# Performance work log

Measured on AMD Instinct MI355X. Metric: run time of the kernel, lower is better.

Reference implementation:

```python
import jax, jax.numpy as jnp
import numpy as np

N_NODES, N_EDGES = 50000, 800000
D_H, D_E, HID = 128, 64, 128  # dim_in = D_H + D_E = 192; hidden_dim2 = D_H + HID = 256


def setup_inputs() -> dict:
    key = jax.random.key(0)
    k1, k2, k3, k4, k5 = jax.random.split(key, 5)
    H = jax.random.normal(k1, (N_NODES, D_H), dtype=jnp.float32)
    idx = jax.random.randint(k2, (2, N_EDGES), 0, N_NODES)
    X_e = jax.random.normal(k3, (N_EDGES, D_E), dtype=jnp.float32)
    # kaiming_normal (fan_in mode, relu gain): std = sqrt(2 / fan_in)
    W1 = jax.random.normal(k4, (D_H + D_E, HID), dtype=jnp.float32) * np.sqrt(2.0 / (D_H + D_E)).astype(np.float32)
    W2 = jax.random.normal(k5, (D_H + HID, HID), dtype=jnp.float32) * np.sqrt(2.0 / (D_H + HID)).astype(np.float32)
    return {"H": H, "idx": idx, "X_e": X_e, "W1": W1, "W2": W2}


def reference(H, idx, X_e, W1, W2):
    # gather source-node embeddings and concat with edge features: [E, d_h + d_e]
    x = jnp.concatenate([H[idx[0]], X_e], axis=1)
    y = jax.nn.relu(x @ W1)                                   # [E, HID]
    # scatter_max into destination nodes; empty segments -> 0 (torch_scatter zero fill).
    y = jax.ops.segment_max(y, idx[1], num_segments=H.shape[0])
    y = jnp.maximum(y, 0.0)  # relu output >= 0, so this only fixes -inf empties
    y = jnp.concatenate([H, y], axis=1)                       # [N, d_h + HID]
    y = jax.nn.relu(y @ W2)                                   # [N, HID]
    return y + H  # residual connection (HID == d_h)
```

## Files before the change

### kernel.cpp

```cpp
#include <hip/hip_runtime.h>
#include <hip/hip_bf16.h>
#include <stdint.h>

#define N_NODES 50000
#define N_EDGES 800000
#define D_H 128
#define D_E 64
#define HID 128

#define MTILE 96
#define SMAX 16
#define N_ETILES ((N_EDGES + MTILE - 1) / MTILE)

#define SCAN_B 512
#define N_CHUNKS ((N_NODES + SCAN_B - 1) / SCAN_B)

typedef __attribute__((ext_vector_type(8))) short bf16x8;
typedef __attribute__((ext_vector_type(4))) short s16x4;
typedef __attribute__((ext_vector_type(4))) float f32x4;
typedef __attribute__((ext_vector_type(4))) int i32x4;

__device__ __forceinline__ unsigned short f2bf(float x) {
    unsigned int u = __float_as_uint(x);
    u += 0x7FFFu + ((u >> 16) & 1u);
    return (unsigned short)(u >> 16);
}

__device__ __forceinline__ bf16x8 pack8(const f32x4 a, const f32x4 b) {
    bf16x8 o = { (short)f2bf(a[0]), (short)f2bf(a[1]), (short)f2bf(a[2]), (short)f2bf(a[3]),
                 (short)f2bf(b[0]), (short)f2bf(b[1]), (short)f2bf(b[2]), (short)f2bf(b[3]) };
    return o;
}

#define NG4 (N_NODES * HID / 4)
#define ND4 (N_NODES / 4)
__global__ void zero_ws(float* __restrict__ gmax, int* __restrict__ deg) {
    const int i = blockIdx.x * blockDim.x + threadIdx.x;
    if (i < NG4) {
        ((f32x4*)gmax)[i] = f32x4{0.f, 0.f, 0.f, 0.f};
    } else if (i < NG4 + ND4) {
        ((i32x4*)deg)[i - NG4] = i32x4{0, 0, 0, 0};
    }
}

#define NHB4 (N_NODES * D_H / 4)
#define NW1 (192 * HID)
#define NW2 (256 * HID)
__global__ void conv_aux(const float* __restrict__ H,
                         const float* __restrict__ W1,
                         const float* __restrict__ W2,
                         unsigned short* __restrict__ Hb,
                         unsigned short* __restrict__ W1t,
                         unsigned short* __restrict__ W2t) {
    const int i = blockIdx.x * blockDim.x + threadIdx.x;
    if (i < NHB4) {
        const f32x4 v = ((const f32x4*)H)[i];
        s16x4 pkv = { (short)f2bf(v[0]), (short)f2bf(v[1]),
                      (short)f2bf(v[2]), (short)f2bf(v[3]) };
        ((s16x4*)Hb)[i] = pkv;
    } else if (i < NHB4 + NW1) {
        const int j = i - NHB4;
        const int n = j / 192, k = j - n * 192;
        W1t[j] = f2bf(W1[k * HID + n]);
    } else if (i < NHB4 + NW1 + NW2) {
        const int j = i - NHB4 - NW1;
        const int n = j >> 8, k = j & 255;
        W2t[j] = f2bf(W2[k * HID + n]);
    }
}

__global__ void hist(const int* __restrict__ idx, int* __restrict__ deg) {
    const int i = blockIdx.x * blockDim.x + threadIdx.x;
    atomicAdd(&deg[idx[N_EDGES + i]], 1);
}

__global__ void scan_a(const int* __restrict__ deg, int* __restrict__ sc,
                       int* __restrict__ totals) {
    __shared__ int s[SCAN_B];
    const int tid = threadIdx.x;
    const int i = blockIdx.x * SCAN_B + tid;
    const int v = (i < N_NODES) ? deg[i] : 0;
    s[tid] = v;
    __syncthreads();
    for (int o = 1; o < SCAN_B; o <<= 1) {
        int t = (tid >= o) ? s[tid - o] : 0;
        __syncthreads();
        s[tid] += t;
        __syncthreads();
    }
    if (i < N_NODES) sc[i] = s[tid] - v;
    if (tid == SCAN_B - 1) totals[blockIdx.x] = s[SCAN_B - 1];
}

__global__ void scan_b(int* __restrict__ totals) {
    __shared__ int s[128];
    const int tid = threadIdx.x;
    const int v = (tid < N_CHUNKS) ? totals[tid] : 0;
    s[tid] = v;
    __syncthreads();
    for (int o = 1; o < 128; o <<= 1) {
        int t = (tid >= o) ? s[tid - o] : 0;
        __syncthreads();
        s[tid] += t;
        __syncthreads();
    }
    if (tid < N_CHUNKS) totals[tid] = s[tid] - v;
}

__global__ void scan_c(const int* __restrict__ sc, const int* __restrict__ totals,
                       int* __restrict__ cursor) {
    const int i = blockIdx.x * SCAN_B + threadIdx.x;
    if (i < N_NODES) cursor[i] = sc[i] + totals[blockIdx.x];
}

__global__ void scatter(const int* __restrict__ idx, int* __restrict__ cursor,
                        unsigned long long* __restrict__ pk8) {
    int i = blockIdx.x * blockDim.x + threadIdx.x;
    const int s = idx[i];
    const int d = idx[N_EDGES + i];
    const int p = atomicAdd(&cursor[d], 1);
    pk8[p] = (unsigned long long)(unsigned)i |
             ((unsigned long long)(unsigned)s << 20) |
             ((unsigned long long)(unsigned)d << 37);
}

__global__ __launch_bounds__(512, 6)
void edge_sorted(const float* __restrict__ H,
                 const unsigned short* __restrict__ Hb,
                 const float* __restrict__ Xe,
                 const float* __restrict__ W1,
                 const unsigned short* __restrict__ W1t,
                 const unsigned long long* __restrict__ pk8,
                 float* __restrict__ gmax, int useAux) {
    __shared__ unsigned short sX[MTILE][200];
    __shared__ float ymax[SMAX + 1][132];
    __shared__ int rowD[MTILE];
    __shared__ int segNode[SMAX];
    __shared__ int sWaveTot[8];
    __shared__ unsigned char rowG[MTILE];

    const int tid  = threadIdx.x;
    const int wave = tid >> 6;
    const int lane = tid & 63;
    const int p0   = blockIdx.x * MTILE;

    const int col = lane & 15;
    const int kr0 = (lane >> 4) * 8;

    if (useAux) {
        #pragma unroll
        for (int it = 0; it < 3; ++it) {
            const int j   = tid + it * 512;
            const int row = j >> 4;
            const int c8  = (j & 15) * 8;
            int pe = p0 + row; if (pe >= N_EDGES) pe = N_EDGES - 1;
            const int src = (int)((pk8[pe] >> 20) & 0x1FFFFull);
            *(bf16x8*)&sX[row][c8] = *(const bf16x8*)(Hb + (size_t)src * D_H + c8);
        }
    } else {
        #pragma unroll
        for (int it = 0; it < 6; ++it) {
            const int j   = tid + it * 512;
            const int row = j >> 5;
            const int c4  = (j & 31) * 4;
            int pe = p0 + row; if (pe >= N_EDGES) pe = N_EDGES - 1;
            const int src = (int)((pk8[pe] >> 20) & 0x1FFFFull);
            const f32x4 v = *(const f32x4*)(H + (size_t)src * D_H + c4);
            s16x4 pkv = { (short)f2bf(v[0]), (short)f2bf(v[1]),
                          (short)f2bf(v[2]), (short)f2bf(v[3]) };
            *(s16x4*)&sX[row][c4] = pkv;
        }
    }
    #pragma unroll
    for (int it = 0; it < 2; ++it) {
        const int j = tid + it * 512;
        if (j < 768) {
            const int row = j >> 3;
            const int c8  = (j & 7) * 8;
            int pe = p0 + row; if (pe >= N_EDGES) pe = N_EDGES - 1;
            const int e = (int)(pk8[pe] & 0xFFFFFull);
            const float* p = Xe + (size_t)e * D_E + c8;
            *(bf16x8*)&sX[row][128 + c8] = pack8(*(const f32x4*)p, *(const f32x4*)(p + 4));
        }
    }

    const int ncol = wave * 16 + col;
    bf16x8 bfrag[6];
    if (useAux) {
        #pragma unroll
        for (int ks = 0; ks < 6; ++ks)
            bfrag[ks] = *(const bf16x8*)&W1t[(size_t)ncol * 192 + ks * 32 + kr0];
    } else {
        #pragma unroll
        for (int ks = 0; ks < 6; ++ks) {
            const int kb = ks * 32 + kr0;
            bf16x8 b;
            #pragma unroll
            for (int f = 0; f < 8; ++f) b[f] = (short)f2bf(W1[(kb + f) * HID + ncol]);
            bfrag[ks] = b;
        }
    }

    const int pe0 = p0 + tid;
    const bool inTile = (tid < MTILE);
    const bool valid  = inTile && (pe0 < N_EDGES);
    int d = 0;
    if (inTile) {
        const int pc = valid ? pe0 : (N_EDGES - 1);
        d = (int)(pk8[pc] >> 37);
        rowD[tid] = d;
    }
    int dp = __shfl_up(d, 1);
    if (lane == 0 && inTile && tid > 0) dp = (int)(pk8[pe0 - 1] >> 37);
    const bool flag = valid && (tid == 0 || d != dp);
    const unsigned long long m = __ballot(flag);
    if (lane == 0) sWaveTot[wave] = (int)__popcll(m);

    for (int i2 = tid; i2 < (SMAX + 1) * 132; i2 += 512) ((float*)ymax)[i2] = 0.f;
    __syncthreads();

    int g = 255;
    if (valid) {
        const unsigned long long le =
            (lane == 63) ? ~0ull : ((1ull << (lane + 1)) - 1);
        g = (int)__popcll(m & le) - 1 + ((wave == 1) ? sWaveTot[0] : 0);
    }
    if (inTile) rowG[tid] = (unsigned char)(valid ? g : 255);
    if (flag && g < SMAX) segNode[g] = d;
    __syncthreads();

    f32x4 acc[6];
    #pragma unroll
    for (int mm = 0; mm < 6; ++mm) acc[mm] = f32x4{0.f, 0.f, 0.f, 0.f};
    const int arow = lane & 15;
    __builtin_amdgcn_s_setprio(1);
    #pragma unroll
    for (int ks = 0; ks < 6; ++ks)
        #pragma unroll
        for (int mm = 0; mm < 6; ++mm) {
            bf16x8 a = *(const bf16x8*)&sX[mm * 16 + arow][ks * 32 + kr0];
            acc[mm] = __builtin_amdgcn_mfma_f32_16x16x32_bf16(a, bfrag[ks], acc[mm], 0, 0, 0);
        }
    __builtin_amdgcn_s_setprio(0);

    const int rb = (lane >> 4) * 4;
    const int cb = wave * 16 + col;
    #pragma unroll
    for (int mm = 0; mm < 6; ++mm) {
        const int r0 = mm * 16 + rb;
        const int g0 = rowG[r0];
        const int g3 = rowG[r0 + 3];
        if (g0 == g3) {
            const float v0 = fmaxf(fmaxf(acc[mm][0], acc[mm][1]),
                                   fmaxf(acc[mm][2], acc[mm][3]));
            if (g0 < SMAX) {
                if (v0 > 0.f) atomicMax((int*)&ymax[g0][cb], __float_as_int(v0));
            } else if (g0 < 255) {
                if (v0 > 0.f)
                    atomicMax((int*)(gmax + (size_t)rowD[r0] * HID + cb), __float_as_int(v0));
            }
        } else {
            #pragma unroll
            for (int r = 0; r < 4; ++r) {
                const int gg = rowG[r0 + r];
                const float v0 = acc[mm][r];
                if (gg < SMAX) {
                    if (v0 > 0.f) atomicMax((int*)&ymax[gg][cb], __float_as_int(v0));
                } else if (gg < 255) {
                    if (v0 > 0.f)
                        atomicMax((int*)(gmax + (size_t)rowD[r0 + r] * HID + cb), __float_as_int(v0));
                }
            }
        }
    }
    __syncthreads();

    const int nSeg = sWaveTot[0] + sWaveTot[1];
    const int nS = (nSeg < SMAX) ? nSeg : SMAX;
    for (int i2 = tid; i2 < nS * 128; i2 += 512) {
        const int sg = i2 >> 7;
        const int c  = i2 & 127;
        const float v = ymax[sg][c];
        float* dst = gmax + (size_t)segNode[sg] * HID + c;
        if (sg == 0 || sg == nSeg - 1) {
            if (v > 0.f) atomicMax((int*)dst, __float_as_int(v));
        } else {
            *dst = v;
        }
    }
}

__global__ __launch_bounds__(256, 4)
void node_mlp(const float* __restrict__ H,
              const float* __restrict__ gmax,
              const float* __restrict__ W2,
              const unsigned short* __restrict__ W2t,
              float* __restrict__ out, int useAux) {
    __shared__ unsigned short sA[64][264];

    const int tid  = threadIdx.x;
    const int wave = tid >> 6;
    const int lane = tid & 63;
    const int base = blockIdx.x * 64;

    const int col = lane & 15;
    const int kr0 = (lane >> 4) * 8;
    bf16x8 bfrag[8][2];
    if (useAux) {
        #pragma unroll
        for (int ks = 0; ks < 8; ++ks)
            #pragma unroll
            for (int nf = 0; nf < 2; ++nf) {
                const int n = wave * 32 + nf * 16 + col;
                bfrag[ks][nf] = *(const bf16x8*)&W2t[(size_t)n * 256 + ks * 32 + kr0];
            }
    } else {
        #pragma unroll
        for (int ks = 0; ks < 8; ++ks)
            #pragma unroll
            for (int nf = 0; nf < 2; ++nf) {
                const int n  = wave * 32 + nf * 16 + col;
                const int kb = ks * 32 + kr0;
                bf16x8 b;
                #pragma unroll
                for (int f = 0; f < 8; ++f) b[f] = (short)f2bf(W2[(kb + f) * HID + n]);
                bfrag[ks][nf] = b;
            }
    }

    #pragma unroll
    for (int it = 0; it < 8; ++it) {
        const int i   = tid + it * 256;
        const int row = i >> 5;
        const int c4  = (i & 31) * 4;
        int node = base + row;
        if (node >= N_NODES) node = N_NODES - 1;
        const f32x4 v = *(const f32x4*)(H + (size_t)node * D_H + c4);
        s16x4 pkv = { (short)f2bf(v[0]), (short)f2bf(v[1]),
                      (short)f2bf(v[2]), (short)f2bf(v[3]) };
        *(s16x4*)&sA[row][c4] = pkv;
    }
    #pragma unroll
    for (int it = 0; it < 8; ++it) {
        const int i   = tid + it * 256;
        const int row = i >> 5;
        const int c4  = (i & 31) * 4;
        int node = base + row;
        if (node >= N_NODES) node = N_NODES - 1;
        const f32x4 v = *(const f32x4*)(gmax + (size_t)node * HID + c4);
        s16x4 pkv = { (short)f2bf(v[0]), (short)f2bf(v[1]),
                      (short)f2bf(v[2]), (short)f2bf(v[3]) };
        *(s16x4*)&sA[row][128 + c4] = pkv;
    }
    __syncthreads();

    f32x4 acc[4][2];
    #pragma unroll
    for (int mm = 0; mm < 4; ++mm) {
        acc[mm][0] = f32x4{0.f, 0.f, 0.f, 0.f};
        acc[mm][1] = f32x4{0.f, 0.f, 0.f, 0.f};
    }
    const int arow = lane & 15;
    __builtin_amdgcn_s_setprio(1);
    #pragma unroll
    for (int ks = 0; ks < 8; ++ks)
        #pragma unroll
        for (int mm = 0; mm < 4; ++mm) {
            bf16x8 a = *(const bf16x8*)&sA[mm * 16 + arow][ks * 32 + kr0];
            acc[mm][0] = __builtin_amdgcn_mfma_f32_16x16x32_bf16(a, bfrag[ks][0], acc[mm][0], 0, 0, 0);
            acc[mm][1] = __builtin_amdgcn_mfma_f32_16x16x32_bf16(a, bfrag[ks][1], acc[mm][1], 0, 0, 0);
        }
    __builtin_amdgcn_s_setprio(0);

    const int rb = (lane >> 4) * 4;
    #pragma unroll
    for (int mm = 0; mm < 4; ++mm)
        #pragma unroll
        for (int r = 0; r < 4; ++r) {
            const int node = base + mm * 16 + rb + r;
            if (node < N_NODES) {
                const size_t o = (size_t)node * HID + wave * 32 + col;
                out[o]      = fmaxf(acc[mm][0][r], 0.f) + H[o];
                out[o + 16] = fmaxf(acc[mm][1][r], 0.f) + H[o + 16];
            }
        }
}

extern "C" void kernel_launch(void* const* d_in, const int* in_sizes, int n_in,
                              void* d_out, int out_size, void* d_ws, size_t ws_size,
                              hipStream_t stream) {
    const float* H   = (const float*)d_in[0];
    const int*   idx = (const int*)d_in[1];
    const float* Xe  = (const float*)d_in[2];
    const float* W1  = (const float*)d_in[3];
    const float* W2  = (const float*)d_in[4];
    float* out = (float*)d_out;

    char* ws = (char*)d_ws;
    float* gmax   = (float*)(ws);
    int*   deg    = (int*)(ws + 25600000);
    int*   sc     = (int*)(ws + 25800192);
    int*   totals = (int*)(ws + 26000384);
    unsigned long long* pk8 = (unsigned long long*)(ws + 26000896);
    unsigned short* W1t = (unsigned short*)(ws + 32400896);
    unsigned short* W2t = (unsigned short*)(ws + 32450048);
    unsigned short* Hb  = (unsigned short*)(ws + 32515584);
    const int useAux = (ws_size >= (size_t)45315584) ? 1 : 0;

    zero_ws<<<(NG4 + ND4 + 255) / 256, 256, 0, stream>>>(gmax, deg);
    if (useAux)
        conv_aux<<<(NHB4 + NW1 + NW2 + 255) / 256, 256, 0, stream>>>(H, W1, W2, Hb, W1t, W2t);
    hist<<<N_EDGES / 256, 256, 0, stream>>>(idx, deg);
    scan_a<<<N_CHUNKS, SCAN_B, 0, stream>>>(deg, sc, totals);
    scan_b<<<1, 128, 0, stream>>>(totals);
    scan_c<<<N_CHUNKS, SCAN_B, 0, stream>>>(sc, totals, deg);
    scatter<<<N_EDGES / 256, 256, 0, stream>>>(idx, deg, pk8);
    edge_sorted<<<N_ETILES, 512, 0, stream>>>(H, Hb, Xe, W1, W1t, pk8, gmax, useAux);
    node_mlp<<<(N_NODES + 63) / 64, 256, 0, stream>>>(H, gmax, W2, W2t, out, useAux);
}
```

Baseline: 258.3 us.

## Make edge kernel persistent over four tiles with register-prefetched gathers

Each edge_sorted block now processes four consecutive 96-edge tiles instead of one. Edge metadata is double-buffered in shared memory, and the gathers of H/Xe rows for the next tile are issued into registers while the current tile's MFMA and scatter-max run. W1 fragment loads and the LDS setup are amortized across tiles. The change adds register pressure (launch bounds lowered to 4 waves per SIMD), extra syncs per tile, and a quarter as many blocks, which may reduce parallelism.

```diff
diff --git a/kernel.cpp b/kernel.cpp
--- a/kernel.cpp
+++ b/kernel.cpp
@@ -11,6 +11,8 @@
 #define MTILE 96
 #define SMAX 16
 #define N_ETILES ((N_EDGES + MTILE - 1) / MTILE)
+#define TPB 4
+#define N_EBLK ((N_ETILES + TPB - 1) / TPB)
 
 #define SCAN_B 512
 #define N_CHUNKS ((N_NODES + SCAN_B - 1) / SCAN_B)
@@ -26,9 +28,9 @@
     return (unsigned short)(u >> 16);
 }
 
-__device__ __forceinline__ bf16x8 pack8(const f32x4 a, const f32x4 b) {
-    bf16x8 o = { (short)f2bf(a[0]), (short)f2bf(a[1]), (short)f2bf(a[2]), (short)f2bf(a[3]),
-                 (short)f2bf(b[0]), (short)f2bf(b[1]), (short)f2bf(b[2]), (short)f2bf(b[3]) };
+__device__ __forceinline__ s16x4 pack4(const f32x4 v) {
+    s16x4 o = { (short)f2bf(v[0]), (short)f2bf(v[1]),
+                (short)f2bf(v[2]), (short)f2bf(v[3]) };
     return o;
 }
 
@@ -54,10 +56,7 @@
                          unsigned short* __restrict__ W2t) {
     const int i = blockIdx.x * blockDim.x + threadIdx.x;
     if (i < NHB4) {
-        const f32x4 v = ((const f32x4*)H)[i];
-        s16x4 pkv = { (short)f2bf(v[0]), (short)f2bf(v[1]),
-                      (short)f2bf(v[2]), (short)f2bf(v[3]) };
-        ((s16x4*)Hb)[i] = pkv;
+        ((s16x4*)Hb)[i] = pack4(((const f32x4*)H)[i]);
     } else if (i < NHB4 + NW1) {
         const int j = i - NHB4;
         const int n = j / 192, k = j - n * 192;
@@ -124,7 +123,7 @@
              ((unsigned long long)(unsigned)d << 37);
 }
 
-__global__ __launch_bounds__(512, 6)
+__global__ __launch_bounds__(512, 4)
 void edge_sorted(const float* __restrict__ H,
                  const unsigned short* __restrict__ Hb,
                  const float* __restrict__ Xe,
@@ -133,8 +132,10 @@
                  const unsigned long long* __restrict__ pk8,
                  float* __restrict__ gmax, int useAux) {
     __shared__ unsigned short sX[MTILE][200];
-    __shared__ float ymax[SMAX + 1][132];
-    __shared__ int rowD[MTILE];
+    __shared__ float ymax[SMAX][132];
+    __shared__ int sMetaE[2][MTILE];
+    __shared__ int sMetaS[2][MTILE];
+    __shared__ int sMetaD[2][MTILE];
     __shared__ int segNode[SMAX];
     __shared__ int sWaveTot[8];
     __shared__ unsigned char rowG[MTILE];
@@ -142,150 +143,184 @@
     const int tid  = threadIdx.x;
     const int wave = tid >> 6;
     const int lane = tid & 63;
-    const int p0   = blockIdx.x * MTILE;
-
-    const int col = lane & 15;
-    const int kr0 = (lane >> 4) * 8;
-
-    if (useAux) {
-        #pragma unroll
-        for (int it = 0; it < 3; ++it) {
-            const int j   = tid + it * 512;
-            const int row = j >> 4;
-            const int c8  = (j & 15) * 8;
-            int pe = p0 + row; if (pe >= N_EDGES) pe = N_EDGES - 1;
-            const int src = (int)((pk8[pe] >> 20) & 0x1FFFFull);
-            *(bf16x8*)&sX[row][c8] = *(const bf16x8*)(Hb + (size_t)src * D_H + c8);
-        }
-    } else {
-        #pragma unroll
-        for (int it = 0; it < 6; ++it) {
-            const int j   = tid + it * 512;
-            const int row = j >> 5;
-            const int c4  = (j & 31) * 4;
-            int pe = p0 + row; if (pe >= N_EDGES) pe = N_EDGES - 1;
-            const int src = (int)((pk8[pe] >> 20) & 0x1FFFFull);
-            const f32x4 v = *(const f32x4*)(H + (size_t)src * D_H + c4);
-            s16x4 pkv = { (short)f2bf(v[0]), (short)f2bf(v[1]),
-                          (short)f2bf(v[2]), (short)f2bf(v[3]) };
-            *(s16x4*)&sX[row][c4] = pkv;
-        }
-    }
-    #pragma unroll
-    for (int it = 0; it < 2; ++it) {
-        const int j = tid + it * 512;
-        if (j < 768) {
-            const int row = j >> 3;
-            const int c8  = (j & 7) * 8;
-            int pe = p0 + row; if (pe >= N_EDGES) pe = N_EDGES - 1;
-            const int e = (int)(pk8[pe] & 0xFFFFFull);
-            const float* p = Xe + (size_t)e * D_E + c8;
-            *(bf16x8*)&sX[row][128 + c8] = pack8(*(const f32x4*)p, *(const f32x4*)(p + 4));
-        }
-    }
-
-    const int ncol = wave * 16 + col;
+    const int t0   = blockIdx.x * TPB;
+    const int nT   = (N_ETILES - t0 < TPB) ? (N_ETILES - t0) : TPB;
+
+    const int col  = lane & 15;
+    const int kr0  = (lane >> 4) * 8;
+    const int arow = lane & 15;
+    const int rb   = (lane >> 4) * 4;
+    const int cb   = wave * 16 + col;
+
     bf16x8 bfrag[6];
     if (useAux) {
         #pragma unroll
         for (int ks = 0; ks < 6; ++ks)
-            bfrag[ks] = *(const bf16x8*)&W1t[(size_t)ncol * 192 + ks * 32 + kr0];
+            bfrag[ks] = *(const bf16x8*)&W1t[(size_t)cb * 192 + ks * 32 + kr0];
     } else {
         #pragma unroll
         for (int ks = 0; ks < 6; ++ks) {
             const int kb = ks * 32 + kr0;
             bf16x8 b;
             #pragma unroll
-            for (int f = 0; f < 8; ++f) b[f] = (short)f2bf(W1[(kb + f) * HID + ncol]);
+            for (int f = 0; f < 8; ++f) b[f] = (short)f2bf(W1[(kb + f) * HID + cb]);
             bfrag[ks] = b;
         }
     }
 
-    const int pe0 = p0 + tid;
-    const bool inTile = (tid < MTILE);
-    const bool valid  = inTile && (pe0 < N_EDGES);
-    int d = 0;
-    if (inTile) {
-        const int pc = valid ? pe0 : (N_EDGES - 1);
-        d = (int)(pk8[pc] >> 37);
-        rowD[tid] = d;
-    }
-    int dp = __shfl_up(d, 1);
-    if (lane == 0 && inTile && tid > 0) dp = (int)(pk8[pe0 - 1] >> 37);
-    const bool flag = valid && (tid == 0 || d != dp);
-    const unsigned long long m = __ballot(flag);
-    if (lane == 0) sWaveTot[wave] = (int)__popcll(m);
-
-    for (int i2 = tid; i2 < (SMAX + 1) * 132; i2 += 512) ((float*)ymax)[i2] = 0.f;
+    for (int i2 = tid; i2 < SMAX * 132; i2 += 512) ((float*)ymax)[i2] = 0.f;
+
+    int dCur = 0, dNext = 0;
+    if (tid < MTILE) {
+        int pe = t0 * MTILE + tid;
+        if (pe >= N_EDGES) pe = N_EDGES - 1;
+        const unsigned long long w = pk8[pe];
+        sMetaE[0][tid] = (int)(w & 0xFFFFFull);
+        sMetaS[0][tid] = (int)((w >> 20) & 0x1FFFFull);
+        sMetaD[0][tid] = (int)(w >> 37);
+        dCur = (int)(w >> 37);
+    }
     __syncthreads();
 
-    int g = 255;
-    if (valid) {
-        const unsigned long long le =
-            (lane == 63) ? ~0ull : ((1ull << (lane + 1)) - 1);
-        g = (int)__popcll(m & le) - 1 + ((wave == 1) ? sWaveTot[0] : 0);
-    }
-    if (inTile) rowG[tid] = (unsigned char)(valid ? g : 255);
-    if (flag && g < SMAX) segNode[g] = d;
-    __syncthreads();
-
-    f32x4 acc[6];
-    #pragma unroll
-    for (int mm = 0; mm < 6; ++mm) acc[mm] = f32x4{0.f, 0.f, 0.f, 0.f};
-    const int arow = lane & 15;
-    __builtin_amdgcn_s_setprio(1);
-    #pragma unroll
-    for (int ks = 0; ks < 6; ++ks)
+    bf16x8 hb[3];
+    f32x4  hraw[6];
+    f32x4  xer[3];
+
+    auto issueGather = [&](int bb) {
+        if (useAux) {
+            #pragma unroll
+            for (int it = 0; it < 3; ++it) {
+                const int j = tid + it * 512, row = j >> 4, c8 = (j & 15) * 8;
+                hb[it] = *(const bf16x8*)(Hb + (size_t)sMetaS[bb][row] * D_H + c8);
+            }
+        } else {
+            #pragma unroll
+            for (int it = 0; it < 6; ++it) {
+                const int j = tid + it * 512, row = j >> 5, c4 = (j & 31) * 4;
+                hraw[it] = *(const f32x4*)(H + (size_t)sMetaS[bb][row] * D_H + c4);
+            }
+        }
+        #pragma unroll
+        for (int it = 0; it < 3; ++it) {
+            const int j = tid + it * 512, row = j >> 4, c4 = (j & 15) * 4;
+            xer[it] = *(const f32x4*)(Xe + (size_t)sMetaE[bb][row] * D_E + c4);
+        }
+    };
+    issueGather(0);
+
+    for (int t = 0; t < nT; ++t) {
+        const int bb = t & 1;
+        const int gt = t0 + t;
+
+        const bool inTile = (tid < MTILE);
+        const bool valid  = inTile && (gt * MTILE + tid < N_EDGES);
+        if (t + 1 < nT && inTile) {
+            int pe = (gt + 1) * MTILE + tid;
+            if (pe >= N_EDGES) pe = N_EDGES - 1;
+            const unsigned long long w = pk8[pe];
+            sMetaE[bb ^ 1][tid] = (int)(w & 0xFFFFFull);
+            sMetaS[bb ^ 1][tid] = (int)((w >> 20) & 0x1FFFFull);
+            sMetaD[bb ^ 1][tid] = (int)(w >> 37);
+            dNext = (int)(w >> 37);
+        }
+        int dp = __shfl_up(dCur, 1);
+        if (lane == 0 && tid == 64) dp = sMetaD[bb][63];
+        const bool flag = valid && (tid == 0 || dCur != dp);
+        const unsigned long long m = __ballot(flag);
+        if (lane == 0) sWaveTot[wave] = (int)__popcll(m);
+
+        if (useAux) {
+            #pragma unroll
+            for (int it = 0; it < 3; ++it) {
+                const int j = tid + it * 512, row = j >> 4, c8 = (j & 15) * 8;
+                *(bf16x8*)&sX[row][c8] = hb[it];
+            }
+        } else {
+            #pragma unroll
+            for (int it = 0; it < 6; ++it) {
+                const int j = tid + it * 512, row = j >> 5, c4 = (j & 31) * 4;
+                *(s16x4*)&sX[row][c4] = pack4(hraw[it]);
+            }
+        }
+        #pragma unroll
+        for (int it = 0; it < 3; ++it) {
+            const int j = tid + it * 512, row = j >> 4, c4 = (j & 15) * 4;
+            *(s16x4*)&sX[row][128 + c4] = pack4(xer[it]);
+        }
+        __syncthreads();
+
+        const int nSegR = sWaveTot[0] + sWaveTot[1];
+        int g = 255;
+        if (valid) {
+            const unsigned long long le =
+                (lane == 63) ? ~0ull : ((1ull << (lane + 1)) - 1);
+            g = (int)__popcll(m & le) - 1 + ((wave == 1) ? sWaveTot[0] : 0);
+        }
+        if (inTile) rowG[tid] = (unsigned char)(valid ? g : 255);
+        if (flag && g < SMAX) segNode[g] = dCur;
+        if (t + 1 < nT) issueGather(bb ^ 1);
+        dCur = dNext;
+        __syncthreads();
+
+        f32x4 acc[6];
+        #pragma unroll
+        for (int mm = 0; mm < 6; ++mm) acc[mm] = f32x4{0.f, 0.f, 0.f, 0.f};
+        __builtin_amdgcn_s_setprio(1);
+        #pragma unroll
+        for (int ks = 0; ks < 6; ++ks)
+            #pragma unroll
+            for (int mm = 0; mm < 6; ++mm) {
+                bf16x8 a = *(const bf16x8*)&sX[mm * 16 + arow][ks * 32 + kr0];
+                acc[mm] = __builtin_amdgcn_mfma_f32_16x16x32_bf16(a, bfrag[ks], acc[mm], 0, 0, 0);
+            }
+        __builtin_amdgcn_s_setprio(0);
+
         #pragma unroll
         for (int mm = 0; mm < 6; ++mm) {
-            bf16x8 a = *(const bf16x8*)&sX[mm * 16 + arow][ks * 32 + kr0];
-            acc[mm] = __builtin_amdgcn_mfma_f32_16x16x32_bf16(a, bfrag[ks], acc[mm], 0, 0, 0);
-        }
-    __builtin_amdgcn_s_setprio(0);
-
-    const int rb = (lane >> 4) * 4;
-    const int cb = wave * 16 + col;
-    #pragma unroll
-    for (int mm = 0; mm < 6; ++mm) {
-        const int r0 = mm * 16 + rb;
-        const int g0 = rowG[r0];
-        const int g3 = rowG[r0 + 3];
-        if (g0 == g3) {
-            const float v0 = fmaxf(fmaxf(acc[mm][0], acc[mm][1]),
-                                   fmaxf(acc[mm][2], acc[mm][3]));
-            if (g0 < SMAX) {
-                if (v0 > 0.f) atomicMax((int*)&ymax[g0][cb], __float_as_int(v0));
-            } else if (g0 < 255) {
-                if (v0 > 0.f)
-                    atomicMax((int*)(gmax + (size_t)rowD[r0] * HID + cb), __float_as_int(v0));
-            }
-        } else {
-            #pragma unroll
-            for (int r = 0; r < 4; ++r) {
-                const int gg = rowG[r0 + r];
-                const float v0 = acc[mm][r];
-                if (gg < SMAX) {
-                    if (v0 > 0.f) atomicMax((int*)&ymax[gg][cb], __float_as_int(v0));
-                } else if (gg < 255) {
+            const int r0 = mm * 16 + rb;
+            const int q0 = rowG[r0];
+            const int q3 = rowG[r0 + 3];
+            if (q0 == q3) {
+                const float v0 = fmaxf(fmaxf(acc[mm][0], acc[mm][1]),
+                                       fmaxf(acc[mm][2], acc[mm][3]));
+                if (q0 < SMAX) {
+                    if (v0 > 0.f) atomicMax((int*)&ymax[q0][cb], __float_as_int(v0));
+                } else if (q0 < 255) {
                     if (v0 > 0.f)
-                        atomicMax((int*)(gmax + (size_t)rowD[r0 + r] * HID + cb), __float_as_int(v0));
+                        atomicMax((int*)(gmax + (size_t)sMetaD[bb][r0] * HID + cb),
+                                  __float_as_int(v0));
                 }
-            }
-        }
-    }
-    __syncthreads();
-
-    const int nSeg = sWaveTot[0] + sWaveTot[1];
-    const int nS = (nSeg < SMAX) ? nSeg : SMAX;
-    for (int i2 = tid; i2 < nS * 128; i2 += 512) {
-        const int sg = i2 >> 7;
-        const int c  = i2 & 127;
-        const float v = ymax[sg][c];
-        float* dst = gmax + (size_t)segNode[sg] * HID + c;
-        if (sg == 0 || sg == nSeg - 1) {
-            if (v > 0.f) atomicMax((int*)dst, __float_as_int(v));
-        } else {
-            *dst = v;
+            } else {
+                #pragma unroll
+                for (int r = 0; r < 4; ++r) {
+                    const int qq = rowG[r0 + r];
+                    const float v0 = acc[mm][r];
+                    if (qq < SMAX) {
+                        if (v0 > 0.f) atomicMax((int*)&ymax[qq][cb], __float_as_int(v0));
+                    } else if (qq < 255) {
+                        if (v0 > 0.f)
+                            atomicMax((int*)(gmax + (size_t)sMetaD[bb][r0 + r] * HID + cb),
+                                      __float_as_int(v0));
+                    }
+                }
+            }
+        }
+        __syncthreads();
+
+        const int nS = (nSegR < SMAX) ? nSegR : SMAX;
+        for (int i2 = tid; i2 < nS * 32; i2 += 512) {
+            const int sg = i2 >> 5;
+            const int c4 = (i2 & 31) * 4;
+            float* dst = gmax + (size_t)segNode[sg] * HID + c4;
+            f32x4 v = *(f32x4*)&ymax[sg][c4];
+            *(f32x4*)&ymax[sg][c4] = f32x4{0.f, 0.f, 0.f, 0.f};
+            if (sg == 0 || sg == nSegR - 1) {
+                #pragma unroll
+                for (int q = 0; q < 4; ++q)
+                    if (v[q] > 0.f) atomicMax((int*)(dst + q), __float_as_int(v[q]));
+            } else {
+                *(f32x4*)dst = v;
+            }
         }
     }
 }
@@ -335,10 +370,7 @@
         const int c4  = (i & 31) * 4;
         int node = base + row;
         if (node >= N_NODES) node = N_NODES - 1;
-        const f32x4 v = *(const f32x4*)(H + (size_t)node * D_H + c4);
-        s16x4 pkv = { (short)f2bf(v[0]), (short)f2bf(v[1]),
-                      (short)f2bf(v[2]), (short)f2bf(v[3]) };
-        *(s16x4*)&sA[row][c4] = pkv;
+        *(s16x4*)&sA[row][c4] = pack4(*(const f32x4*)(H + (size_t)node * D_H + c4));
     }
     #pragma unroll
     for (int it = 0; it < 8; ++it) {
@@ -347,10 +379,7 @@
         const int c4  = (i & 31) * 4;
         int node = base + row;
         if (node >= N_NODES) node = N_NODES - 1;
-        const f32x4 v = *(const f32x4*)(gmax + (size_t)node * HID + c4);
-        s16x4 pkv = { (short)f2bf(v[0]), (short)f2bf(v[1]),
-                      (short)f2bf(v[2]), (short)f2bf(v[3]) };
-        *(s16x4*)&sA[row][128 + c4] = pkv;
+        *(s16x4*)&sA[row][128 + c4] = pack4(*(const f32x4*)(gmax + (size_t)node * HID + c4));
     }
     __syncthreads();
 
@@ -415,6 +444,6 @@
     scan_b<<<1, 128, 0, stream>>>(totals);
     scan_c<<<N_CHUNKS, SCAN_B, 0, stream>>>(sc, totals, deg);
     scatter<<<N_EDGES / 256, 256, 0, stream>>>(idx, deg, pk8);
-    edge_sorted<<<N_ETILES, 512, 0, stream>>>(H, Hb, Xe, W1, W1t, pk8, gmax, useAux);
+    edge_sorted<<<N_EBLK, 512, 0, stream>>>(H, Hb, Xe, W1, W1t, pk8, gmax, useAux);
     node_mlp<<<(N_NODES + 63) / 64, 256, 0, stream>>>(H, gmax, W2, W2t, out, useAux);
 }
```

Result: slower. 318.6 us (+23.4%).
